# Kernel optimization log

Measured on AMD Instinct MI355X. Metric: run time of the kernel, lower is better.

Reference implementation:

```python
import jax, jax.numpy as jnp
import numpy as np

# --- problem sizes (fixed channel widths come from the module's irreps arithmetic) ---
N, E = 100000, 1600000
NUM_ELEM, F0, RB, HID = 4, 4, 10, 10          # len(atomic_list), embedding_dim[0], embedding_dim[1], hidden_dim
EDGE_DIM, SH_DIM = 2 * F0 + RB, 9             # 18, lmax=2 -> 1+3+5
GATE_IN, GATE_OUT = 92, 76                    # 12 scalars + 16 gates + 64 gated ; 12 + 64
CUTOFF, P_ENV, AVG_DEG = 5.0, 6, 16.0


def setup_inputs() -> dict:
    key = jax.random.key(0)
    ks = jax.random.split(key, 16)
    d = {}
    d["type_indices"] = jax.random.randint(ks[0], (N,), 0, NUM_ELEM)
    d["positions"] = jax.random.uniform(ks[1], (N, 3), dtype=jnp.float32) * 6.0
    # radius_graph replaced by a fixed-size random edge list (jit-friendly, same downstream math)
    d["edge_src"] = jax.random.randint(ks[2], (E,), 0, N)
    d["edge_dest"] = jax.random.randint(ks[3], (E,), 0, N)
    d["embed_table"] = jax.random.normal(ks[4], (NUM_ELEM, F0), dtype=jnp.float32)
    fins = [F0, GATE_OUT, GATE_OUT]
    fouts = [GATE_IN, GATE_IN, 1]
    for i in range(3):
        d[f"mlp{i+1}_w1"] = jax.random.normal(ks[5 + 3 * i], (EDGE_DIM, HID), dtype=jnp.float32) / np.float32(np.sqrt(EDGE_DIM))
        d[f"mlp{i+1}_w2"] = jax.random.normal(ks[6 + 3 * i], (HID, SH_DIM), dtype=jnp.float32) / np.float32(np.sqrt(HID))
        d[f"tp{i+1}"] = jax.random.normal(ks[7 + 3 * i], (SH_DIM, fins[i], fouts[i]), dtype=jnp.float32) / np.float32(np.sqrt(fins[i]))
    return d


def sph_harmonics(vec):
    # real spherical harmonics up to l=2, 'component' normalization, on normalized vectors
    r = jnp.linalg.norm(vec, axis=-1, keepdims=True)
    u = vec / jnp.maximum(r, 1e-9)
    x, y, z = u[:, 0], u[:, 1], u[:, 2]
    c1 = np.float32(np.sqrt(3.0))
    c2 = np.float32(np.sqrt(15.0))
    c2b = np.float32(np.sqrt(5.0) / 2.0)
    return jnp.stack([
        jnp.ones_like(x),
        c1 * y, c1 * z, c1 * x,
        c2 * x * y, c2 * y * z, c2b * (3.0 * z * z - 1.0), c2 * x * z, (c2 / 2.0) * (x * x - y * y),
    ], axis=-1)  # [E, 9]


def radial_embed(r):
    # Bessel radial basis with DimeNet-style polynomial envelope (p=6)
    x = r / CUTOFF                                    # [E, 1]
    n = jnp.arange(1, RB + 1, dtype=jnp.float32)      # [RB]
    bess = np.float32(np.sqrt(2.0 / CUTOFF)) * jnp.sin(n * jnp.pi * x) / jnp.maximum(r, 1e-9)
    p = P_ENV
    env = (1.0 - (p + 1) * (p + 2) / 2.0 * x ** p + p * (p + 2) * x ** (p + 1) - p * (p + 1) / 2.0 * x ** (p + 2))
    return bess * env                                 # [E, RB]


def gate(x):
    # e3nn Gate: scalars 4x0e(relu)+8x0o(abs), gates 4x0e(relu)+4x0o(tanh)+4x0e(relu)+4x0o(tanh),
    # gated irreps 4x1o+4x1e (3 comps each) + 4x2e+4x2o (5 comps each)
    s, g, v = x[:, :12], x[:, 12:28], x[:, 28:]
    s_act = jnp.concatenate([jax.nn.relu(s[:, :4]), jnp.abs(s[:, 4:])], axis=-1)
    g_act = jnp.concatenate([jax.nn.relu(g[:, 0:4]), jnp.tanh(g[:, 4:8]),
                             jax.nn.relu(g[:, 8:12]), jnp.tanh(g[:, 12:16])], axis=-1)
    g_exp = jnp.concatenate([jnp.repeat(g_act[:, :8], 3, axis=1),   # 8 gates x 3 comps (l=1)
                             jnp.repeat(g_act[:, 8:], 5, axis=1)],  # 8 gates x 5 comps (l=2)
                            axis=-1)                                 # [*, 64]
    return jnp.concatenate([s_act, v * g_exp], axis=-1)             # [*, 76]


def conv(x, edge_src, edge_dest, sh, edge_embed, w1, w2, tp):
    # per-edge weights from 2-layer MLP on edge embedding, one weight per SH component (factorized TP)
    w = jax.nn.relu(edge_embed @ w1) @ w2             # [E, 9]
    shw = sh * w                                      # [E, 9]
    xg = x[edge_src]                                  # gather [E, F_in]
    msg = shw[:, 0:1] * (xg @ tp[0])
    for s in range(1, SH_DIM):                        # fixed small loop over SH components
        msg = msg + shw[:, s:s + 1] * (xg @ tp[s])
    out = jax.ops.segment_sum(msg, edge_dest, num_segments=x.shape[0])
    return out / np.float32(np.sqrt(AVG_DEG))


def reference(type_indices, positions, edge_src, edge_dest, embed_table,
              mlp1_w1, mlp1_w2, tp1, mlp2_w1, mlp2_w2, tp2, mlp3_w1, mlp3_w2, tp3):
    te = embed_table[type_indices]                            # [N, 4]
    ev = positions[edge_dest] - positions[edge_src]           # [E, 3]
    el = jnp.linalg.norm(ev, axis=-1, keepdims=True)          # [E, 1]
    ee = jnp.concatenate([te[edge_dest], te[edge_src], radial_embed(el)], axis=-1)  # [E, 18]
    sh = sph_harmonics(ev)                                    # [E, 9]
    x0 = te
    x1 = gate(conv(x0, edge_src, edge_dest, sh, ee, mlp1_w1, mlp1_w2, tp1))
    x1 = x1.at[:, :F0].add(x0)                                # scalar-channel residual
    x2 = gate(conv(x1, edge_src, edge_dest, sh, ee, mlp2_w1, mlp2_w2, tp2)) + x1
    x3 = conv(x2, edge_src, edge_dest, sh, ee, mlp3_w1, mlp3_w2, tp3)  # [N, 1]
    return jnp.sum(x3)
```

## Files before the change

kernel.cpp:

```cpp
#include <hip/hip_runtime.h>
#include <hip/hip_bf16.h>
#include <math.h>

typedef unsigned int uint32;
typedef __attribute__((ext_vector_type(8))) short short8;
typedef __attribute__((ext_vector_type(4))) float f32x4;

#define TBINS 1024
#define RMAX  10.4f
#define BSHIFT 7
#define BDR    (1<<BSHIFT)

__device__ __forceinline__ uint32 pack_bf16(float a, float b){
  __hip_bfloat16 ba = __float2bfloat16(a);
  __hip_bfloat16 bb = __float2bfloat16(b);
  unsigned short ua = *reinterpret_cast<unsigned short*>(&ba);
  unsigned short ub = *reinterpret_cast<unsigned short*>(&bb);
  return (uint32)ua | ((uint32)ub << 16);
}
__device__ __forceinline__ float bf_lo(uint32 u){ return __uint_as_float(u << 16); }
__device__ __forceinline__ float bf_hi(uint32 u){ return __uint_as_float(u & 0xffff0000u); }


__global__ __launch_bounds__(1024) void k_bcount(
    const int* __restrict__ esrc, const int* __restrict__ edst,
    int* __restrict__ gb1, int* __restrict__ gb2, int E){
  __shared__ int c1[1024], c2[1024];
  int tid = threadIdx.x;
  c1[tid] = 0; c2[tid] = 0;
  __syncthreads();
  int e0 = blockIdx.x * 8192;
  #pragma unroll
  for (int k=0;k<8;k++){
    int e = e0 + k*1024 + tid;
    if (e < E){
      atomicAdd(&c1[edst[e] >> BSHIFT], 1);
      atomicAdd(&c2[esrc[e] >> BSHIFT], 1);
    }
  }
  __syncthreads();
  if (c1[tid]) atomicAdd(&gb1[tid], c1[tid]);
  if (c2[tid]) atomicAdd(&gb2[tid], c2[tid]);
}


__global__ __launch_bounds__(1024) void k_bscan(
    const int* __restrict__ gb1, const int* __restrict__ gb2,
    int* __restrict__ boff1, int* __restrict__ boff2,
    int* __restrict__ gcur1, int* __restrict__ gcur2,
    int* __restrict__ offsets, int* __restrict__ off2,
    int N, int E, int NBUCK){
  __shared__ int sm[1024];
  int tid = threadIdx.x;
  int v = (tid < NBUCK) ? gb1[tid] : 0;
  sm[tid] = v; __syncthreads();
  for (int off=1; off<1024; off<<=1){
    int t = (tid >= off) ? sm[tid-off] : 0;
    __syncthreads();
    sm[tid] += t;
    __syncthreads();
  }
  if (tid < NBUCK){ int o = sm[tid]-v; boff1[tid] = o; gcur1[tid] = o; }
  __syncthreads();
  int v2 = (tid < NBUCK) ? gb2[tid] : 0;
  sm[tid] = v2; __syncthreads();
  for (int off=1; off<1024; off<<=1){
    int t = (tid >= off) ? sm[tid-off] : 0;
    __syncthreads();
    sm[tid] += t;
    __syncthreads();
  }
  if (tid < NBUCK){ int o = sm[tid]-v2; boff2[tid] = o; gcur2[tid] = o; }
  if (tid == 0){
    boff1[NBUCK] = E; boff2[NBUCK] = E;
    offsets[N] = E;   off2[N] = E;
  }
}


__global__ __launch_bounds__(1024) void k_binA(
    const int* __restrict__ key, const int* __restrict__ pay,
    int* __restrict__ gcur, int2* __restrict__ pair, int E, int NBUCK){
  __shared__ int cnt[1024];
  __shared__ int run[1024];
  int tid = threadIdx.x;
  int e0 = blockIdx.x * 8192;
  cnt[tid] = 0;
  __syncthreads();
  #pragma unroll
  for (int k=0;k<8;k++){
    int e = e0 + k*1024 + tid;
    if (e < E) atomicAdd(&cnt[key[e] >> BSHIFT], 1);
  }
  __syncthreads();
  if (tid < NBUCK && cnt[tid] > 0) run[tid] = atomicAdd(&gcur[tid], cnt[tid]);
  __syncthreads();
  #pragma unroll
  for (int k=0;k<8;k++){
    int e = e0 + k*1024 + tid;
    if (e < E){
      int kk = key[e];
      int p = atomicAdd(&run[kk >> BSHIFT], 1);
      int2 pr; pr.x = pay[e]; pr.y = kk;
      pair[p] = pr;
    }
  }
}


__global__ __launch_bounds__(256) void k_binB2(
    const int2* __restrict__ pair, const int* __restrict__ boff,
    int* __restrict__ offsets, int* __restrict__ csr_out, int N){
  __shared__ int cnt[BDR];
  __shared__ int scn[BDR];
  int base = blockIdx.x << BSHIFT;
  int hi = base + BDR; if (hi > N) hi = N;
  int nloc = hi - base;
  if (nloc <= 0) return;
  int tid = threadIdx.x;
  if (tid < BDR) cnt[tid] = 0;
  __syncthreads();
  int p0 = boff[blockIdx.x], p1 = boff[blockIdx.x+1];
  for (int p = p0 + tid; p < p1; p += 256) atomicAdd(&cnt[pair[p].y - base], 1);
  __syncthreads();
  int val = (tid < BDR) ? cnt[tid] : 0;
  if (tid < BDR) scn[tid] = val;
  __syncthreads();
  for (int off=1; off<BDR; off<<=1){
    int t = (tid >= off && tid < BDR) ? scn[tid-off] : 0;
    __syncthreads();
    if (tid < BDR) scn[tid] += t;
    __syncthreads();
  }
  if (tid < nloc){
    int o = p0 + scn[tid] - val;
    offsets[base + tid] = o;
    cnt[tid] = o;
  }
  __syncthreads();
  for (int p = p0 + tid; p < p1; p += 256){
    int2 pr = pair[p];
    int slot = atomicAdd(&cnt[pr.y - base], 1);
    csr_out[slot] = pr.x;
  }
}


__global__ void k_pack(const float* __restrict__ pos, const int* __restrict__ types,
                       float4* __restrict__ ptyp, int N){
  int i = blockIdx.x*256 + threadIdx.x;
  if (i >= N) return;
  float4 f; f.x = pos[3*i]; f.y = pos[3*i+1]; f.z = pos[3*i+2]; f.w = __int_as_float(types[i]);
  ptyp[i] = f;
}


__device__ __forceinline__ void radial_mlp(
    float r, int td, int ts, const float* sEmb,
    const float* sW1, const float* sW2, float* w_out ){
  float ee[18];
  #pragma unroll
  for (int i=0;i<4;i++){ ee[i] = sEmb[td*4+i]; ee[4+i] = sEmb[ts*4+i]; }
  float rm = fmaxf(r, 1e-9f);
  float inv = 1.f/rm;
  float xx = r * 0.2f;
  float x2v = xx*xx, x3v = x2v*xx, x6 = x3v*x3v, x7 = x6*xx, x8 = x7*xx;
  float env = 1.f - 28.f*x6 + 48.f*x7 - 21.f*x8;
  const float bc = 0.6324555320336759f;
  float pref = bc * env * inv;
  const float PI = 3.14159265358979323846f;
  float s1, cth;
  __sincosf(PI*xx, &s1, &cth);
  float two_c = 2.f*cth;
  float sp = 0.f, sc = s1;
  ee[8] = pref * sc;
  #pragma unroll
  for (int n=2;n<=10;n++){
    float sn = two_c*sc - sp;
    sp = sc; sc = sn;
    ee[7+n] = pref * sc;
  }
  float h[10];
  #pragma unroll
  for (int j=0;j<10;j++){
    float a = 0.f;
    #pragma unroll
    for (int k=0;k<18;k++) a = fmaf(ee[k], sW1[k*10+j], a);
    h[j] = fmaxf(a, 0.f);
  }
  #pragma unroll
  for (int sj=0;sj<9;sj++){
    float a = 0.f;
    #pragma unroll
    for (int j=0;j<10;j++) a = fmaf(h[j], sW2[j*9+sj], a);
    w_out[sj] = a;
  }
}


__global__ __launch_bounds__(256) void k_mktab(
    const float* __restrict__ embed,
    const float* __restrict__ w1a, const float* __restrict__ w2a,
    const float* __restrict__ w1b, const float* __restrict__ w2b,
    const float* __restrict__ w1c, const float* __restrict__ w2c,
    uint32* __restrict__ tab){
  __shared__ float sEmb[16];
  __shared__ float sW1a[180], sW2a[90], sW1b[180], sW2b[90], sW1c[180], sW2c[90];
  int t = threadIdx.x;
  if (t < 16) sEmb[t] = embed[t];
  if (t < 180){ sW1a[t] = w1a[t]; sW1b[t] = w1b[t]; sW1c[t] = w1c[t]; }
  if (t < 90){  sW2a[t] = w2a[t]; sW2b[t] = w2b[t]; sW2c[t] = w2c[t]; }
  __syncthreads();
  int gid = blockIdx.x*256 + t;
  if (gid >= 16*TBINS) return;
  int combo = gid / TBINS, bin = gid - combo*TBINS;
  int td = combo >> 2, ts = combo & 3;
  const float dR = RMAX / TBINS;
  float r0 = bin*dR, r1 = r0 + dR;
  float a0[9], a1[9], b0[9], b1[9], c0[9], c1[9];
  radial_mlp(r0, td, ts, sEmb, sW1a, sW2a, a0);
  radial_mlp(r1, td, ts, sEmb, sW1a, sW2a, a1);
  radial_mlp(r0, td, ts, sEmb, sW1b, sW2b, b0);
  radial_mlp(r1, td, ts, sEmb, sW1b, sW2b, b1);
  radial_mlp(r0, td, ts, sEmb, sW1c, sW2c, c0);
  radial_mlp(r1, td, ts, sEmb, sW1c, sW2c, c1);
  uint32* rec = tab + (size_t)gid*32;
  #pragma unroll
  for (int s=0;s<9;s++){
    rec[s]    = pack_bf16(a0[s], a1[s]-a0[s]);
    rec[9+s]  = pack_bf16(b0[s], b1[s]-b0[s]);
    rec[18+s] = pack_bf16(c0[s], c1[s]-c0[s]);
  }
  #pragma unroll
  for (int s=27;s<32;s++) rec[s] = 0u;
}


__global__ __launch_bounds__(256) void k_layer12t(
    const int* __restrict__ offsets, const int* __restrict__ csr_src,
    const float4* __restrict__ ptyp, const float* __restrict__ embed,
    const uint32* __restrict__ tab, const float* __restrict__ tp1,
    float* __restrict__ x1, uint32* __restrict__ shwb, int N){
  __shared__ float sT[36*92];
  __shared__ float sEmb[16];
  int t = threadIdx.x;
  if (t < 16) sEmb[t] = embed[t];
  for (int i=t; i<36*92; i+=256) sT[i] = tp1[i]*0.25f;
  __syncthreads();
  int gid = blockIdx.x*256 + t;
  int n = gid >> 2, q = gid & 3;
  if (n >= N) return;
  float4 fd = ptyp[n];
  float dx = fd.x, dy = fd.y, dz = fd.z;
  int td = __float_as_int(fd.w);
  const float c1 = 1.7320508075688772f, c2 = 3.872983346207417f, c2b = 1.118033988749895f;
  const float invD = (float)TBINS / RMAX;
  float Z[36];
  #pragma unroll
  for (int i=0;i<36;i++) Z[i]=0.f;
  int b0 = offsets[n], b1 = offsets[n+1];
  for (int j=b0+q; j<b1; j+=4){
    int s = csr_src[j];
    float4 fs = ptyp[s];
    float px = dx - fs.x, py = dy - fs.y, pz = dz - fs.z;
    int ts_ = __float_as_int(fs.w);
    float r = sqrtf(px*px + py*py + pz*pz);
    float inv = 1.f/fmaxf(r, 1e-9f);
    float ux = px*inv, uy = py*inv, uz = pz*inv;
    float sh[9];
    sh[0]=1.f; sh[1]=c1*uy; sh[2]=c1*uz; sh[3]=c1*ux;
    sh[4]=c2*ux*uy; sh[5]=c2*uy*uz; sh[6]=c2b*(3.f*uz*uz-1.f); sh[7]=c2*ux*uz;
    sh[8]=0.5f*c2*(ux*ux-uy*uy);
    float tt = r * invD;
    int bb = (int)tt; bb = (bb > TBINS-1) ? TBINS-1 : bb;
    float frac = tt - (float)bb;
    const uint32* rec = tab + ((size_t)((td*4+ts_)*TBINS + bb))*32;
    uint32 R[20];
    #pragma unroll
    for (int i=0;i<5;i++) *(uint4*)&R[i*4] = *(const uint4*)(rec + i*4);
    float x0[4];
    #pragma unroll
    for (int i=0;i<4;i++) x0[i] = sEmb[ts_*4+i];
    float sw2[9];
    #pragma unroll
    for (int sj=0;sj<9;sj++){
      uint32 ua = R[sj], ub = R[9+sj];
      float w1v = fmaf(frac, bf_hi(ua), bf_lo(ua));
      float w2v = fmaf(frac, bf_hi(ub), bf_lo(ub));
      float s1v = sh[sj]*w1v;
      sw2[sj] = sh[sj]*w2v;
      #pragma unroll
      for (int i=0;i<4;i++) Z[sj*4+i] = fmaf(s1v, x0[i], Z[sj*4+i]);
    }
    uint32* so = shwb + (size_t)j*5;
    so[0]=pack_bf16(sw2[0],sw2[1]); so[1]=pack_bf16(sw2[2],sw2[3]);
    so[2]=pack_bf16(sw2[4],sw2[5]); so[3]=pack_bf16(sw2[6],sw2[7]);
    so[4]=pack_bf16(sw2[8],0.f);
  }
  #pragma unroll
  for (int m=1; m<=2; m<<=1){
    #pragma unroll
    for (int i=0;i<36;i++) Z[i] += __shfl_xor(Z[i], m, 4);
  }
  float* xo = x1 + (size_t)n*76;
  int gi_prev = -1; float ga = 0.f;
  for (int cc=q*19; cc<q*19+19; cc++){
    float v;
    if (cc < 12){
      float y = 0.f;
      #pragma unroll
      for (int p=0;p<36;p++) y = fmaf(Z[p], sT[p*92+cc], y);
      v = (cc<4) ? (fmaxf(y,0.f) + sEmb[td*4+cc]) : fabsf(y);
    } else {
      int j = cc - 12;
      int gi = (j<24) ? (j/3) : (8 + (j-24)/5);
      if (gi != gi_prev){
        float gy = 0.f;
        #pragma unroll
        for (int p=0;p<36;p++) gy = fmaf(Z[p], sT[p*92+12+gi], gy);
        ga = (gi<4 || (gi>=8 && gi<12)) ? fmaxf(gy,0.f) : tanhf(gy);
        gi_prev = gi;
      }
      float y = 0.f;
      #pragma unroll
      for (int p=0;p<36;p++) y = fmaf(Z[p], sT[p*92+28+j], y);
      v = y*ga;
    }
    xo[cc] = v;
  }
}


__global__ void k_cast(const float* __restrict__ x1, uint32* __restrict__ x1b, int n38){
  int i = blockIdx.x*256 + threadIdx.x;
  if (i >= n38) return;
  float2 f = *(const float2*)&x1[(size_t)i*2];
  x1b[i] = pack_bf16(f.x, f.y);
}


__global__ __launch_bounds__(256) void k_conv2c(
    const int* __restrict__ offsets, const int* __restrict__ csr_src,
    const uint32* __restrict__ shwb, const uint32* __restrict__ x1b,
    uint32* __restrict__ Z2u, int d0, int dend){
  int g = blockIdx.x*256 + threadIdx.x;
  int dg = g/38;
  int u = g - dg*38;
  int d = d0 + dg;
  if (d >= dend) return;
  float z[9], zb[9];
  #pragma unroll
  for (int s=0;s<9;s++){ z[s]=0.f; zb[s]=0.f; }
  int b0 = offsets[d], b1 = offsets[d+1];
  for (int j=b0;j<b1;j++){
    int sn = csr_src[j];
    uint32 xv = x1b[(size_t)sn*38 + u];
    float xa = bf_lo(xv), xb = bf_hi(xv);
    const uint32* sw = shwb + (size_t)j*5;
    uint32 a0=sw[0], a1=sw[1], a2=sw[2], a3=sw[3], a4=sw[4];
    float w[9];
    w[0]=bf_lo(a0); w[1]=bf_hi(a0); w[2]=bf_lo(a1); w[3]=bf_hi(a1);
    w[4]=bf_lo(a2); w[5]=bf_hi(a2); w[6]=bf_lo(a3); w[7]=bf_hi(a3); w[8]=bf_lo(a4);
    #pragma unroll
    for (int s=0;s<9;s++){
      z[s]  = fmaf(w[s], xa, z[s]);
      zb[s] = fmaf(w[s], xb, zb[s]);
    }
  }
  uint32* zr = Z2u + (size_t)dg*352;
  #pragma unroll
  for (int s=0;s<9;s++) zr[s*38+u] = pack_bf16(z[s], zb[s]);
  if (u < 10) zr[342+u] = 0u;
}


__global__ void k_wprep2(const float* __restrict__ tp2, unsigned short* __restrict__ Wt){
  int q = blockIdx.x*256 + threadIdx.x;
  if (q >= 22*96*32) return;
  int kin = q & 31;
  int rest = q >> 5;
  int col = rest % 96, s = rest / 96;
  int k = s*32 + kin;
  float v = (k < 684 && col < 92) ? tp2[k*92+col]*0.25f : 0.f;
  __hip_bfloat16 b = __float2bfloat16(v);
  Wt[q] = *reinterpret_cast<unsigned short*>(&b);
}


__global__ __launch_bounds__(256) void k_gemm2m(
    const uint32* __restrict__ Z2u, const unsigned short* __restrict__ Wt,
    const float* __restrict__ x1, const float* __restrict__ tp3,
    float* __restrict__ A, int d0, int dend){
  __shared__ float lw[64][100];
  __shared__ float tl3[684];
  int t = threadIdx.x;
  for (int i=t;i<684;i+=256) tl3[i] = tp3[i]*0.25f;
  int w = t >> 6, l = t & 63;
  int lrow = l & 15, lk = l >> 4;
  int mb = blockIdx.x*64;
  const uint32* arow = Z2u + (size_t)(mb + w*16 + lrow)*352 + lk*4;
  const short8* bb = (const short8*)Wt;
  int boff = lrow*4 + lk;
  f32x4 acc[6];
  #pragma unroll
  for (int ct=0;ct<6;ct++) acc[ct] = (f32x4){0.f,0.f,0.f,0.f};
  for (int s=0;s<22;s++){
    short8 af = *(const short8*)(arow + s*16);
    #pragma unroll
    for (int ct=0;ct<6;ct++){
      short8 bf = bb[(s*96 + ct*16)*4 + boff];
      acc[ct] = __builtin_amdgcn_mfma_f32_16x16x32_bf16(af, bf, acc[ct], 0, 0, 0);
    }
  }
  #pragma unroll
  for (int ct=0;ct<6;ct++)
    #pragma unroll
    for (int i=0;i<4;i++)
      lw[w*16 + lk*4 + i][ct*16 + lrow] = acc[ct][i];
  __syncthreads();
  int m = t>>2, q = t&3;
  int node = d0 + mb + m;
  float pA[9];
  #pragma unroll
  for (int s=0;s<9;s++) pA[s]=0.f;
  if (node < dend){
    const float* xr = x1 + (size_t)node*76;
    for (int cc=q*19; cc<q*19+19; cc++){
      float v;
      if (cc < 12){
        float y = lw[m][cc];
        v = (cc<4) ? fmaxf(y,0.f) : fabsf(y);
      } else {
        int j = cc-12;
        int gi = (j<24) ? (j/3) : (8 + (j-24)/5);
        float gy = lw[m][12+gi];
        float ga = (gi<4 || (gi>=8 && gi<12)) ? fmaxf(gy,0.f) : tanhf(gy);
        v = lw[m][28+j]*ga;
      }
      float xv = v + xr[cc];
      #pragma unroll
      for (int s=0;s<9;s++) pA[s] = fmaf(xv, tl3[s*76+cc], pA[s]);
    }
  }
  #pragma unroll
  for (int off=1; off<=2; off<<=1){
    #pragma unroll
    for (int s=0;s<9;s++) pA[s] += __shfl_xor(pA[s], off, 4);
  }
  if (node < dend && q == 0){
    float* Ar = A + (size_t)node*16;
    float4 w0 = {pA[0],pA[1],pA[2],pA[3]};
    float4 w1 = {pA[4],pA[5],pA[6],pA[7]};
    *(float4*)Ar = w0;
    *(float4*)(Ar+4) = w1;
    Ar[8] = pA[8];
  }
}


__global__ __launch_bounds__(256) void k_g3t(
    const int* __restrict__ off2, const int* __restrict__ csr2_dst,
    const float4* __restrict__ ptyp, const uint32* __restrict__ tab,
    float* __restrict__ G, int N){
  int gid = blockIdx.x*256 + threadIdx.x;
  int n = gid >> 2, q = gid & 3;
  if (n >= N) return;
  float acc[9];
  #pragma unroll
  for (int s=0;s<9;s++) acc[s]=0.f;
  float4 fs = ptyp[n];
  float sx = fs.x, sy = fs.y, sz = fs.z;
  int ts_ = __float_as_int(fs.w);
  const float c1 = 1.7320508075688772f, c2 = 3.872983346207417f, c2b = 1.118033988749895f;
  const float invD = (float)TBINS / RMAX;
  int b0 = off2[n], b1 = off2[n+1];
  for (int j=b0+q; j<b1; j+=4){
    int d = csr2_dst[j];
    float4 fdd = ptyp[d];
    float px = fdd.x-sx, py = fdd.y-sy, pz = fdd.z-sz;
    int td_ = __float_as_int(fdd.w);
    float r = sqrtf(px*px + py*py + pz*pz);
    float inv = 1.f/fmaxf(r, 1e-9f);
    float ux = px*inv, uy = py*inv, uz = pz*inv;
    float sh[9];
    sh[0]=1.f; sh[1]=c1*uy; sh[2]=c1*uz; sh[3]=c1*ux;
    sh[4]=c2*ux*uy; sh[5]=c2*uy*uz; sh[6]=c2b*(3.f*uz*uz-1.f); sh[7]=c2*ux*uz;
    sh[8]=0.5f*c2*(ux*ux-uy*uy);
    float tt = r * invD;
    int bb = (int)tt; bb = (bb > TBINS-1) ? TBINS-1 : bb;
    float frac = tt - (float)bb;
    const uint32* rec = tab + ((size_t)((td_*4+ts_)*TBINS + bb))*32;
    uint32 R[12];
    #pragma unroll
    for (int i=0;i<3;i++) *(uint4*)&R[i*4] = *(const uint4*)(rec + 16 + i*4);
    #pragma unroll
    for (int sj=0;sj<9;sj++){
      uint32 u = R[2+sj];
      float w = fmaf(frac, bf_hi(u), bf_lo(u));
      acc[sj] = fmaf(sh[sj], w, acc[sj]);
    }
  }
  #pragma unroll
  for (int off=2; off>0; off>>=1){
    #pragma unroll
    for (int s=0;s<9;s++) acc[s] += __shfl_down(acc[s], off, 4);
  }
  if (q == 0){
    float* gr = G + (size_t)n*12;
    float4 w0 = {acc[0],acc[1],acc[2],acc[3]};
    float4 w1 = {acc[4],acc[5],acc[6],acc[7]};
    *(float4*)gr = w0;
    *(float4*)(gr+4) = w1;
    gr[8] = acc[8];
  }
}


__global__ __launch_bounds__(256) void k_finalG(
    const float* __restrict__ G, const float* __restrict__ A,
    float* __restrict__ out, int N){
  int n = blockIdx.x*256 + threadIdx.x;
  float part = 0.f;
  if (n < N){
    const float* gr = G + (size_t)n*12;
    const float* Ar = A + (size_t)n*16;
    float4 g0 = *(const float4*)gr, g1 = *(const float4*)(gr+4);
    float4 a0 = *(const float4*)Ar, a1 = *(const float4*)(Ar+4);
    part = g0.x*a0.x + g0.y*a0.y + g0.z*a0.z + g0.w*a0.w
         + g1.x*a1.x + g1.y*a1.y + g1.z*a1.z + g1.w*a1.w
         + gr[8]*Ar[8];
  }
  #pragma unroll
  for (int off=32; off>0; off>>=1) part += __shfl_down(part, off, 64);
  if ((threadIdx.x & 63) == 0) atomicAdd(out, part);
}


extern "C" void kernel_launch(void* const* d_in, const int* in_sizes, int n_in,
                              void* d_out, int out_size, void* d_ws, size_t ws_size,
                              hipStream_t stream){
  const int*   types = (const int*)d_in[0];
  const float* pos   = (const float*)d_in[1];
  const int*   esrc  = (const int*)d_in[2];
  const int*   edst  = (const int*)d_in[3];
  const float* embed = (const float*)d_in[4];
  const float* m1w1=(const float*)d_in[5],  *m1w2=(const float*)d_in[6],  *tp1=(const float*)d_in[7];
  const float* m2w1=(const float*)d_in[8],  *m2w2=(const float*)d_in[9],  *tp2=(const float*)d_in[10];
  const float* m3w1=(const float*)d_in[11], *m3w2=(const float*)d_in[12], *tp3=(const float*)d_in[13];
  int N = in_sizes[0];
  int E = in_sizes[2];
  float* out = (float*)d_out;

  char* wsb = (char*)d_ws; size_t off = 0;
  auto alloc = [&](size_t b)->char*{ char* p = wsb + off; off = (off + b + 255) & ~(size_t)255; return p; };
  float*  x1      = (float*)alloc((size_t)N*76*sizeof(float));
  uint32* x1b     = (uint32*)alloc((size_t)N*38*sizeof(uint32));
  float4* ptyp    = (float4*)alloc((size_t)N*sizeof(float4));
  uint32* shwb    = (uint32*)alloc((size_t)E*5*sizeof(uint32));
  int*    csr_src = (int*)alloc((size_t)E*sizeof(int));
  int*    csr2_dst= (int*)alloc((size_t)E*sizeof(int));
  int2*   pair    = (int2*)alloc((size_t)E*sizeof(int2));
  int*    offsets = (int*)alloc((size_t)(N+1)*sizeof(int));
  int*    off2    = (int*)alloc((size_t)(N+1)*sizeof(int));
  int*    gb1     = (int*)alloc(1024*sizeof(int));
  int*    gb2     = (int*)alloc(1024*sizeof(int));
  int*    boff1   = (int*)alloc(1025*sizeof(int));
  int*    boff2   = (int*)alloc(1025*sizeof(int));
  int*    gcur1   = (int*)alloc(1024*sizeof(int));
  int*    gcur2   = (int*)alloc(1024*sizeof(int));
  unsigned short* Wt = (unsigned short*)alloc((size_t)22*96*32*sizeof(unsigned short));
  float*  A       = (float*)alloc((size_t)N*16*sizeof(float));
  float*  G       = (float*)alloc((size_t)N*12*sizeof(float));
  uint32* tab     = (uint32*)alloc((size_t)16*TBINS*32*sizeof(uint32));

  size_t avail = (ws_size > off) ? (ws_size - off - 512) : 0;
  long long rows = (long long)(avail / (352*sizeof(uint32))) - 64;
  int CH = (rows > 50176) ? 50176 : (int)rows;
  CH = (CH / 64) * 64;
  if (CH < 64) CH = 64;
  uint32* Z2u = (uint32*)alloc((size_t)(CH+64)*352*sizeof(uint32));

  hipMemsetAsync(gb1, 0, 2048*sizeof(int), stream);
  hipMemsetAsync(out, 0, sizeof(float), stream);

  int nbE = (E+255)/256;
  int nbN = (N+255)/256;
  int nbT = (16*TBINS+255)/256;
  int NBUCK = (N + BDR - 1) >> BSHIFT;
  int nbC = (E+8191)/8192;
  k_pack<<<nbN,256,0,stream>>>(pos, types, ptyp, N);
  k_mktab<<<nbT,256,0,stream>>>(embed, m1w1, m1w2, m2w1, m2w2, m3w1, m3w2, tab);
  k_bcount<<<nbC,1024,0,stream>>>(esrc, edst, gb1, gb2, E);
  k_bscan<<<1,1024,0,stream>>>(gb1, gb2, boff1, boff2, gcur1, gcur2,
                               offsets, off2, N, E, NBUCK);
  k_binA<<<nbC,1024,0,stream>>>(edst, esrc, gcur1, pair, E, NBUCK);
  k_binB2<<<NBUCK,256,0,stream>>>(pair, boff1, offsets, csr_src, N);
  k_binA<<<nbC,1024,0,stream>>>(esrc, edst, gcur2, pair, E, NBUCK);
  k_binB2<<<NBUCK,256,0,stream>>>(pair, boff2, off2, csr2_dst, N);

  k_wprep2<<<(22*96*32+255)/256,256,0,stream>>>(tp2, Wt);

  k_g3t<<<(4*N+255)/256,256,0,stream>>>(off2, csr2_dst, ptyp, tab, G, N);

  k_layer12t<<<(4*N+255)/256,256,0,stream>>>(offsets, csr_src, ptyp, embed,
                                             tab, tp1, x1, shwb, N);
  k_cast<<<(N*38+255)/256,256,0,stream>>>(x1, x1b, N*38);

  for (int d0 = 0; d0 < N; d0 += CH){
    int dend = (d0 + CH < N) ? (d0 + CH) : N;
    int nn = dend - d0;
    k_conv2c<<<((nn*38)+255)/256,256,0,stream>>>(offsets, csr_src, shwb, x1b, Z2u, d0, dend);
    k_gemm2m<<<(nn+63)/64,256,0,stream>>>(Z2u, Wt, x1, tp3, A, d0, dend);
  }

  k_finalG<<<nbN,256,0,stream>>>(G, A, out, N);
}
```

Baseline: 495.6 us.

## Switch edge kernels to edge-parallel blocks with shared-memory atomic accumulation

Layer-1 and G kernels now assign one thread per edge within a 64-node block. Each thread finds its destination node by binary search over local offsets and accumulates into shared memory with atomics, instead of four threads per node looping over neighbours. Layer 1 also accumulates per-source-type SH-weighted sums (36 floats per node) and applies the embedding afterwards, removing the per-edge 36-FMA inner product. This targets load imbalance from variable node degree. The cost is LDS atomic contention and binary-search overhead.

Measured after the change: 616.1 us. 1.24x slower.

```diff
diff --git a/kernel.cpp b/kernel.cpp
--- a/kernel.cpp
+++ b/kernel.cpp
@@ -236,33 +236,37 @@
 }
 
 
-__global__ __launch_bounds__(256) void k_layer12t(
+__global__ __launch_bounds__(256) void k_edgeA(
     const int* __restrict__ offsets, const int* __restrict__ csr_src,
     const float4* __restrict__ ptyp, const float* __restrict__ embed,
     const uint32* __restrict__ tab, const float* __restrict__ tp1,
     float* __restrict__ x1, uint32* __restrict__ shwb, int N){
   __shared__ float sT[36*92];
   __shared__ float sEmb[16];
+  __shared__ float S[64*36];
+  __shared__ int loff[65];
   int t = threadIdx.x;
+  int n0 = blockIdx.x*64;
+  int nloc = N - n0; if (nloc > 64) nloc = 64;
+  if (nloc <= 0) return;
   if (t < 16) sEmb[t] = embed[t];
   for (int i=t; i<36*92; i+=256) sT[i] = tp1[i]*0.25f;
-  __syncthreads();
-  int gid = blockIdx.x*256 + t;
-  int n = gid >> 2, q = gid & 3;
-  if (n >= N) return;
-  float4 fd = ptyp[n];
-  float dx = fd.x, dy = fd.y, dz = fd.z;
-  int td = __float_as_int(fd.w);
+  for (int i=t; i<64*36; i+=256) S[i] = 0.f;
+  for (int i=t; i<=64; i+=256) loff[i] = offsets[n0 + (i<nloc ? i : nloc)];
+  __syncthreads();
   const float c1 = 1.7320508075688772f, c2 = 3.872983346207417f, c2b = 1.118033988749895f;
   const float invD = (float)TBINS / RMAX;
-  float Z[36];
-  #pragma unroll
-  for (int i=0;i<36;i++) Z[i]=0.f;
-  int b0 = offsets[n], b1 = offsets[n+1];
-  for (int j=b0+q; j<b1; j+=4){
+  int p0 = loff[0], p1 = loff[64];
+  for (int j = p0 + t; j < p1; j += 256){
+    int lo = 0, hi = 64;
+    #pragma unroll
+    for (int it=0; it<6; it++){ int mid = (lo+hi)>>1; if (loff[mid] <= j) lo = mid; else hi = mid; }
+    int d = lo;
+    float4 fd = ptyp[n0+d];
+    int td = __float_as_int(fd.w);
     int s = csr_src[j];
     float4 fs = ptyp[s];
-    float px = dx - fs.x, py = dy - fs.y, pz = dz - fs.z;
+    float px = fd.x - fs.x, py = fd.y - fs.y, pz = fd.z - fs.z;
     int ts_ = __float_as_int(fs.w);
     float r = sqrtf(px*px + py*py + pz*pz);
     float inv = 1.f/fmaxf(r, 1e-9f);
@@ -278,30 +282,37 @@
     uint32 R[20];
     #pragma unroll
     for (int i=0;i<5;i++) *(uint4*)&R[i*4] = *(const uint4*)(rec + i*4);
-    float x0[4];
-    #pragma unroll
-    for (int i=0;i<4;i++) x0[i] = sEmb[ts_*4+i];
+    float* Sd = &S[d*36 + ts_*9];
     float sw2[9];
     #pragma unroll
     for (int sj=0;sj<9;sj++){
       uint32 ua = R[sj], ub = R[9+sj];
       float w1v = fmaf(frac, bf_hi(ua), bf_lo(ua));
       float w2v = fmaf(frac, bf_hi(ub), bf_lo(ub));
-      float s1v = sh[sj]*w1v;
       sw2[sj] = sh[sj]*w2v;
-      #pragma unroll
-      for (int i=0;i<4;i++) Z[sj*4+i] = fmaf(s1v, x0[i], Z[sj*4+i]);
+      atomicAdd(&Sd[sj], sh[sj]*w1v);
     }
     uint32* so = shwb + (size_t)j*5;
     so[0]=pack_bf16(sw2[0],sw2[1]); so[1]=pack_bf16(sw2[2],sw2[3]);
     so[2]=pack_bf16(sw2[4],sw2[5]); so[3]=pack_bf16(sw2[6],sw2[7]);
     so[4]=pack_bf16(sw2[8],0.f);
   }
-  #pragma unroll
-  for (int m=1; m<=2; m<<=1){
-    #pragma unroll
-    for (int i=0;i<36;i++) Z[i] += __shfl_xor(Z[i], m, 4);
-  }
+  __syncthreads();
+  int d = t >> 2, q = t & 3;
+  if (d >= nloc) return;
+  int n = n0 + d;
+  int td = __float_as_int(ptyp[n].w);
+  float Z[36];
+  const float* Sd = &S[d*36];
+  #pragma unroll
+  for (int sj=0;sj<9;sj++)
+    #pragma unroll
+    for (int i=0;i<4;i++){
+      float z = 0.f;
+      #pragma unroll
+      for (int t4=0;t4<4;t4++) z = fmaf(sEmb[t4*4+i], Sd[t4*9+sj], z);
+      Z[sj*4+i] = z;
+    }
   float* xo = x1 + (size_t)n*76;
   int gi_prev = -1; float ga = 0.f;
   for (int cc=q*19; cc<q*19+19; cc++){
@@ -331,6 +342,65 @@
 }
 
 
+__global__ __launch_bounds__(256) void k_edgeB(
+    const int* __restrict__ off2, const int* __restrict__ csr2_dst,
+    const float4* __restrict__ ptyp, const uint32* __restrict__ tab,
+    float* __restrict__ G, int N){
+  __shared__ float Gl[64*4*9];
+  __shared__ int loff[65];
+  int t = threadIdx.x;
+  int n0 = blockIdx.x*64;
+  int nloc = N - n0; if (nloc > 64) nloc = 64;
+  if (nloc <= 0) return;
+  for (int i=t; i<64*4*9; i+=256) Gl[i] = 0.f;
+  for (int i=t; i<=64; i+=256) loff[i] = off2[n0 + (i<nloc ? i : nloc)];
+  __syncthreads();
+  const float c1 = 1.7320508075688772f, c2 = 3.872983346207417f, c2b = 1.118033988749895f;
+  const float invD = (float)TBINS / RMAX;
+  int p0 = loff[0], p1 = loff[64];
+  int slot = t & 3;
+  for (int j = p0 + t; j < p1; j += 256){
+    int lo = 0, hi = 64;
+    #pragma unroll
+    for (int it=0; it<6; it++){ int mid = (lo+hi)>>1; if (loff[mid] <= j) lo = mid; else hi = mid; }
+    int d = lo;
+    float4 fs = ptyp[n0+d];
+    int ts_ = __float_as_int(fs.w);
+    int dd = csr2_dst[j];
+    float4 fdd = ptyp[dd];
+    float px = fdd.x - fs.x, py = fdd.y - fs.y, pz = fdd.z - fs.z;
+    int td_ = __float_as_int(fdd.w);
+    float r = sqrtf(px*px + py*py + pz*pz);
+    float inv = 1.f/fmaxf(r, 1e-9f);
+    float ux = px*inv, uy = py*inv, uz = pz*inv;
+    float sh[9];
+    sh[0]=1.f; sh[1]=c1*uy; sh[2]=c1*uz; sh[3]=c1*ux;
+    sh[4]=c2*ux*uy; sh[5]=c2*uy*uz; sh[6]=c2b*(3.f*uz*uz-1.f); sh[7]=c2*ux*uz;
+    sh[8]=0.5f*c2*(ux*ux-uy*uy);
+    float tt = r * invD;
+    int bb = (int)tt; bb = (bb > TBINS-1) ? TBINS-1 : bb;
+    float frac = tt - (float)bb;
+    const uint32* rec = tab + ((size_t)((td_*4+ts_)*TBINS + bb))*32;
+    uint32 R[12];
+    #pragma unroll
+    for (int i=0;i<3;i++) *(uint4*)&R[i*4] = *(const uint4*)(rec + 16 + i*4);
+    float* Gd = &Gl[(d*4+slot)*9];
+    #pragma unroll
+    for (int sj=0;sj<9;sj++){
+      uint32 u = R[2+sj];
+      float w = fmaf(frac, bf_hi(u), bf_lo(u));
+      atomicAdd(&Gd[sj], sh[sj]*w);
+    }
+  }
+  __syncthreads();
+  for (int i=t; i<nloc*9; i+=256){
+    int d = i/9, sj = i - d*9;
+    float g = Gl[(d*4+0)*9+sj] + Gl[(d*4+1)*9+sj] + Gl[(d*4+2)*9+sj] + Gl[(d*4+3)*9+sj];
+    G[(size_t)(n0+d)*12 + sj] = g;
+  }
+}
+
+
 __global__ void k_cast(const float* __restrict__ x1, uint32* __restrict__ x1b, int n38){
   int i = blockIdx.x*256 + threadIdx.x;
   if (i >= n38) return;
@@ -454,64 +524,6 @@
     *(float4*)Ar = w0;
     *(float4*)(Ar+4) = w1;
     Ar[8] = pA[8];
-  }
-}
-
-
-__global__ __launch_bounds__(256) void k_g3t(
-    const int* __restrict__ off2, const int* __restrict__ csr2_dst,
-    const float4* __restrict__ ptyp, const uint32* __restrict__ tab,
-    float* __restrict__ G, int N){
-  int gid = blockIdx.x*256 + threadIdx.x;
-  int n = gid >> 2, q = gid & 3;
-  if (n >= N) return;
-  float acc[9];
-  #pragma unroll
-  for (int s=0;s<9;s++) acc[s]=0.f;
-  float4 fs = ptyp[n];
-  float sx = fs.x, sy = fs.y, sz = fs.z;
-  int ts_ = __float_as_int(fs.w);
-  const float c1 = 1.7320508075688772f, c2 = 3.872983346207417f, c2b = 1.118033988749895f;
-  const float invD = (float)TBINS / RMAX;
-  int b0 = off2[n], b1 = off2[n+1];
-  for (int j=b0+q; j<b1; j+=4){
-    int d = csr2_dst[j];
-    float4 fdd = ptyp[d];
-    float px = fdd.x-sx, py = fdd.y-sy, pz = fdd.z-sz;
-    int td_ = __float_as_int(fdd.w);
-    float r = sqrtf(px*px + py*py + pz*pz);
-    float inv = 1.f/fmaxf(r, 1e-9f);
-    float ux = px*inv, uy = py*inv, uz = pz*inv;
-    float sh[9];
-    sh[0]=1.f; sh[1]=c1*uy; sh[2]=c1*uz; sh[3]=c1*ux;
-    sh[4]=c2*ux*uy; sh[5]=c2*uy*uz; sh[6]=c2b*(3.f*uz*uz-1.f); sh[7]=c2*ux*uz;
-    sh[8]=0.5f*c2*(ux*ux-uy*uy);
-    float tt = r * invD;
-    int bb = (int)tt; bb = (bb > TBINS-1) ? TBINS-1 : bb;
-    float frac = tt - (float)bb;
-    const uint32* rec = tab + ((size_t)((td_*4+ts_)*TBINS + bb))*32;
-    uint32 R[12];
-    #pragma unroll
-    for (int i=0;i<3;i++) *(uint4*)&R[i*4] = *(const uint4*)(rec + 16 + i*4);
-    #pragma unroll
-    for (int sj=0;sj<9;sj++){
-      uint32 u = R[2+sj];
-      float w = fmaf(frac, bf_hi(u), bf_lo(u));
-      acc[sj] = fmaf(sh[sj], w, acc[sj]);
-    }
-  }
-  #pragma unroll
-  for (int off=2; off>0; off>>=1){
-    #pragma unroll
-    for (int s=0;s<9;s++) acc[s] += __shfl_down(acc[s], off, 4);
-  }
-  if (q == 0){
-    float* gr = G + (size_t)n*12;
-    float4 w0 = {acc[0],acc[1],acc[2],acc[3]};
-    float4 w1 = {acc[4],acc[5],acc[6],acc[7]};
-    *(float4*)gr = w0;
-    *(float4*)(gr+4) = w1;
-    gr[8] = acc[8];
   }
 }
 
@@ -583,8 +595,8 @@
   hipMemsetAsync(gb1, 0, 2048*sizeof(int), stream);
   hipMemsetAsync(out, 0, sizeof(float), stream);
 
-  int nbE = (E+255)/256;
   int nbN = (N+255)/256;
+  int nbB = (N+63)/64;
   int nbT = (16*TBINS+255)/256;
   int NBUCK = (N + BDR - 1) >> BSHIFT;
   int nbC = (E+8191)/8192;
@@ -600,10 +612,9 @@
 
   k_wprep2<<<(22*96*32+255)/256,256,0,stream>>>(tp2, Wt);
 
-  k_g3t<<<(4*N+255)/256,256,0,stream>>>(off2, csr2_dst, ptyp, tab, G, N);
-
-  k_layer12t<<<(4*N+255)/256,256,0,stream>>>(offsets, csr_src, ptyp, embed,
-                                             tab, tp1, x1, shwb, N);
+  k_edgeB<<<nbB,256,0,stream>>>(off2, csr2_dst, ptyp, tab, G, N);
+
+  k_edgeA<<<nbB,256,0,stream>>>(offsets, csr_src, ptyp, embed, tab, tp1, x1, shwb, N);
   k_cast<<<(N*38+255)/256,256,0,stream>>>(x1, x1b, N*38);
 
   for (int d0 = 0; d0 < N; d0 += CH){
```

## Fuse both edge binning passes into one kernel and store SH weights planar

Applied to the files above, without the earlier changes.

Merges the two k_binA launches into a single k_binA2 that reads esrc/edst once and bins edges into two separate pair buffers for the dst-sorted and src-sorted CSR builds. This removes one full pass over the edge arrays and one launch, at the cost of an extra E-sized pair buffer and doubled shared-memory atomics per block. It also changes the per-edge SH-weight buffer from a 5-word interleaved record to five planar E-length arrays. Writes from k_layer12t and reads in k_conv2c become strided by E per component rather than contiguous per edge. Within a warp, consecutive lanes touch consecutive edges in each plane, which could coalesce better.

Result: no change. 499.4 us (+0.8%).

```diff
diff --git a/kernel.cpp b/kernel.cpp
--- a/kernel.cpp
+++ b/kernel.cpp
@@ -78,31 +78,41 @@
 }
 
 
-__global__ __launch_bounds__(1024) void k_binA(
-    const int* __restrict__ key, const int* __restrict__ pay,
-    int* __restrict__ gcur, int2* __restrict__ pair, int E, int NBUCK){
-  __shared__ int cnt[1024];
-  __shared__ int run[1024];
+__global__ __launch_bounds__(1024) void k_binA2(
+    const int* __restrict__ esrc, const int* __restrict__ edst,
+    int* __restrict__ gcur1, int* __restrict__ gcur2,
+    int2* __restrict__ pair1, int2* __restrict__ pair2, int E, int NBUCK){
+  __shared__ int cnt1[1024], run1[1024];
+  __shared__ int cnt2[1024], run2[1024];
   int tid = threadIdx.x;
   int e0 = blockIdx.x * 8192;
-  cnt[tid] = 0;
-  __syncthreads();
-  #pragma unroll
-  for (int k=0;k<8;k++){
-    int e = e0 + k*1024 + tid;
-    if (e < E) atomicAdd(&cnt[key[e] >> BSHIFT], 1);
-  }
-  __syncthreads();
-  if (tid < NBUCK && cnt[tid] > 0) run[tid] = atomicAdd(&gcur[tid], cnt[tid]);
+  cnt1[tid] = 0; cnt2[tid] = 0;
   __syncthreads();
   #pragma unroll
   for (int k=0;k<8;k++){
     int e = e0 + k*1024 + tid;
     if (e < E){
-      int kk = key[e];
-      int p = atomicAdd(&run[kk >> BSHIFT], 1);
-      int2 pr; pr.x = pay[e]; pr.y = kk;
-      pair[p] = pr;
+      atomicAdd(&cnt1[edst[e] >> BSHIFT], 1);
+      atomicAdd(&cnt2[esrc[e] >> BSHIFT], 1);
+    }
+  }
+  __syncthreads();
+  if (tid < NBUCK){
+    if (cnt1[tid] > 0) run1[tid] = atomicAdd(&gcur1[tid], cnt1[tid]);
+    if (cnt2[tid] > 0) run2[tid] = atomicAdd(&gcur2[tid], cnt2[tid]);
+  }
+  __syncthreads();
+  #pragma unroll
+  for (int k=0;k<8;k++){
+    int e = e0 + k*1024 + tid;
+    if (e < E){
+      int s = esrc[e], d = edst[e];
+      int p1 = atomicAdd(&run1[d >> BSHIFT], 1);
+      int2 pr1; pr1.x = s; pr1.y = d;
+      pair1[p1] = pr1;
+      int p2 = atomicAdd(&run2[s >> BSHIFT], 1);
+      int2 pr2; pr2.x = d; pr2.y = s;
+      pair2[p2] = pr2;
     }
   }
 }
@@ -240,7 +250,7 @@
     const int* __restrict__ offsets, const int* __restrict__ csr_src,
     const float4* __restrict__ ptyp, const float* __restrict__ embed,
     const uint32* __restrict__ tab, const float* __restrict__ tp1,
-    float* __restrict__ x1, uint32* __restrict__ shwb, int N){
+    float* __restrict__ x1, uint32* __restrict__ shwb, int N, int E){
   __shared__ float sT[36*92];
   __shared__ float sEmb[16];
   int t = threadIdx.x;
@@ -292,10 +302,11 @@
       #pragma unroll
       for (int i=0;i<4;i++) Z[sj*4+i] = fmaf(s1v, x0[i], Z[sj*4+i]);
     }
-    uint32* so = shwb + (size_t)j*5;
-    so[0]=pack_bf16(sw2[0],sw2[1]); so[1]=pack_bf16(sw2[2],sw2[3]);
-    so[2]=pack_bf16(sw2[4],sw2[5]); so[3]=pack_bf16(sw2[6],sw2[7]);
-    so[4]=pack_bf16(sw2[8],0.f);
+    shwb[j]             = pack_bf16(sw2[0],sw2[1]);
+    shwb[(size_t)E+j]   = pack_bf16(sw2[2],sw2[3]);
+    shwb[(size_t)2*E+j] = pack_bf16(sw2[4],sw2[5]);
+    shwb[(size_t)3*E+j] = pack_bf16(sw2[6],sw2[7]);
+    shwb[(size_t)4*E+j] = pack_bf16(sw2[8],0.f);
   }
   #pragma unroll
   for (int m=1; m<=2; m<<=1){
@@ -342,7 +353,7 @@
 __global__ __launch_bounds__(256) void k_conv2c(
     const int* __restrict__ offsets, const int* __restrict__ csr_src,
     const uint32* __restrict__ shwb, const uint32* __restrict__ x1b,
-    uint32* __restrict__ Z2u, int d0, int dend){
+    uint32* __restrict__ Z2u, int d0, int dend, int E){
   int g = blockIdx.x*256 + threadIdx.x;
   int dg = g/38;
   int u = g - dg*38;
@@ -356,8 +367,11 @@
     int sn = csr_src[j];
     uint32 xv = x1b[(size_t)sn*38 + u];
     float xa = bf_lo(xv), xb = bf_hi(xv);
-    const uint32* sw = shwb + (size_t)j*5;
-    uint32 a0=sw[0], a1=sw[1], a2=sw[2], a3=sw[3], a4=sw[4];
+    uint32 a0 = shwb[j];
+    uint32 a1 = shwb[(size_t)E+j];
+    uint32 a2 = shwb[(size_t)2*E+j];
+    uint32 a3 = shwb[(size_t)3*E+j];
+    uint32 a4 = shwb[(size_t)4*E+j];
     float w[9];
     w[0]=bf_lo(a0); w[1]=bf_hi(a0); w[2]=bf_lo(a1); w[3]=bf_hi(a1);
     w[4]=bf_lo(a2); w[5]=bf_hi(a2); w[6]=bf_lo(a3); w[7]=bf_hi(a3); w[8]=bf_lo(a4);
@@ -559,7 +573,8 @@
   uint32* shwb    = (uint32*)alloc((size_t)E*5*sizeof(uint32));
   int*    csr_src = (int*)alloc((size_t)E*sizeof(int));
   int*    csr2_dst= (int*)alloc((size_t)E*sizeof(int));
-  int2*   pair    = (int2*)alloc((size_t)E*sizeof(int2));
+  int2*   pair1   = (int2*)alloc((size_t)E*sizeof(int2));
+  int2*   pair2   = (int2*)alloc((size_t)E*sizeof(int2));
   int*    offsets = (int*)alloc((size_t)(N+1)*sizeof(int));
   int*    off2    = (int*)alloc((size_t)(N+1)*sizeof(int));
   int*    gb1     = (int*)alloc(1024*sizeof(int));
@@ -583,7 +598,6 @@
   hipMemsetAsync(gb1, 0, 2048*sizeof(int), stream);
   hipMemsetAsync(out, 0, sizeof(float), stream);
 
-  int nbE = (E+255)/256;
   int nbN = (N+255)/256;
   int nbT = (16*TBINS+255)/256;
   int NBUCK = (N + BDR - 1) >> BSHIFT;
@@ -593,23 +607,22 @@
   k_bcount<<<nbC,1024,0,stream>>>(esrc, edst, gb1, gb2, E);
   k_bscan<<<1,1024,0,stream>>>(gb1, gb2, boff1, boff2, gcur1, gcur2,
                                offsets, off2, N, E, NBUCK);
-  k_binA<<<nbC,1024,0,stream>>>(edst, esrc, gcur1, pair, E, NBUCK);
-  k_binB2<<<NBUCK,256,0,stream>>>(pair, boff1, offsets, csr_src, N);
-  k_binA<<<nbC,1024,0,stream>>>(esrc, edst, gcur2, pair, E, NBUCK);
-  k_binB2<<<NBUCK,256,0,stream>>>(pair, boff2, off2, csr2_dst, N);
+  k_binA2<<<nbC,1024,0,stream>>>(esrc, edst, gcur1, gcur2, pair1, pair2, E, NBUCK);
+  k_binB2<<<NBUCK,256,0,stream>>>(pair1, boff1, offsets, csr_src, N);
+  k_binB2<<<NBUCK,256,0,stream>>>(pair2, boff2, off2, csr2_dst, N);
 
   k_wprep2<<<(22*96*32+255)/256,256,0,stream>>>(tp2, Wt);
 
   k_g3t<<<(4*N+255)/256,256,0,stream>>>(off2, csr2_dst, ptyp, tab, G, N);
 
   k_layer12t<<<(4*N+255)/256,256,0,stream>>>(offsets, csr_src, ptyp, embed,
-                                             tab, tp1, x1, shwb, N);
+                                             tab, tp1, x1, shwb, N, E);
   k_cast<<<(N*38+255)/256,256,0,stream>>>(x1, x1b, N*38);
 
   for (int d0 = 0; d0 < N; d0 += CH){
     int dend = (d0 + CH < N) ? (d0 + CH) : N;
     int nn = dend - d0;
-    k_conv2c<<<((nn*38)+255)/256,256,0,stream>>>(offsets, csr_src, shwb, x1b, Z2u, d0, dend);
+    k_conv2c<<<((nn*38)+255)/256,256,0,stream>>>(offsets, csr_src, shwb, x1b, Z2u, d0, dend, E);
     k_gemm2m<<<(nn+63)/64,256,0,stream>>>(Z2u, Wt, x1, tp3, A, d0, dend);
   }
 
```
